# Kernel optimization log

Hardware: AMD Instinct MI355X
Metric: run time of the kernel (lower is better)

## Reference

```python
import jax, jax.numpy as jnp
import numpy as np

B, S, H, NH = 4, 2048, 2048, 16
HD = H // NH
EPS = 1e-5


def setup_inputs() -> dict:
    key = jax.random.key(0)
    ks = jax.random.split(key, 5)
    return {
        "x": jax.random.normal(ks[0], (B, S, H), dtype=jnp.float32),
        "ln_w": jnp.ones((H,), dtype=jnp.float32),
        "ln_b": jnp.zeros((H,), dtype=jnp.float32),
        "c_attn_w": jax.random.normal(ks[1], (H, 3 * H), dtype=jnp.float32) * 0.02,
        "c_attn_b": jax.random.normal(ks[2], (3 * H,), dtype=jnp.float32) * 0.02,
        "c_proj_w": jax.random.normal(ks[3], (H, H), dtype=jnp.float32) * 0.02,
        "c_proj_b": jax.random.normal(ks[4], (H,), dtype=jnp.float32) * 0.02,
    }


def reference(x, ln_w, ln_b, c_attn_w, c_attn_b, c_proj_w, c_proj_b):
    residual = x
    # fused layer norm
    mu = jnp.mean(x, axis=-1, keepdims=True)
    var = jnp.mean(jnp.square(x - mu), axis=-1, keepdims=True)
    xn = (x - mu) * jax.lax.rsqrt(var + EPS) * ln_w + ln_b
    qkv = jnp.einsum("bsh,hk->bsk", xn, c_attn_w) + c_attn_b
    q, k, v = jnp.split(qkv, 3, axis=-1)
    def heads(t):
        return t.reshape(B, S, NH, HD).transpose(0, 2, 1, 3)
    q, k, v = heads(q), heads(k), heads(v)
    # causal flash attention (reference math)
    scale = 1.0 / np.sqrt(HD)
    scores = jnp.einsum("bnqd,bnkd->bnqk", q, k) * scale
    causal = jnp.tril(jnp.ones((S, S), dtype=bool))
    scores = jnp.where(causal, scores, jnp.finfo(scores.dtype).min)
    attn = jax.nn.softmax(scores, axis=-1)
    o = jnp.einsum("bnqk,bnkd->bnqd", attn, v)
    # merge heads: [B,NH,S,HD] -> [B,S,H]
    o = o.transpose(0, 2, 1, 3).reshape(B, S, H)
    # output projection + residual (fused_ffn, add_gelu=False, dropout=0)
    return jnp.einsum("bsh,hk->bsk", o, c_proj_w) + c_proj_b + residual
```

## Files before the change

### kernel.cpp

```cpp
#include <hip/hip_runtime.h>
#include <stdint.h>
#include <math.h>

#define B_  4
#define S_  2048
#define H_  2048
#define NH_ 16
#define HD_ 128
#define M_  (B_*S_)
#define N3_ (3*H_)
#define NQT_ (S_/64)

typedef __attribute__((ext_vector_type(8))) short short8;
typedef __attribute__((ext_vector_type(4))) float floatx4;
typedef unsigned int u32;

__device__ __forceinline__ unsigned short f2bf(float f) {
  unsigned u = __float_as_uint(f);
  u += 0x7FFF + ((u >> 16) & 1);
  return (unsigned short)(u >> 16);
}

__device__ __forceinline__ void gl2lds16(const void* g, void* l) {
  __builtin_amdgcn_global_load_lds(
      (const __attribute__((address_space(1))) u32*)g,
      (__attribute__((address_space(3))) u32*)l, 16, 0, 0);
}

__global__ __launch_bounds__(256) void ln_kernel(
    const float* __restrict__ x, const float* __restrict__ w,
    const float* __restrict__ b, unsigned short* __restrict__ xn) {
  int row = blockIdx.x;
  int t = threadIdx.x;
  const float* xr = x + (size_t)row * H_;
  float4 v0 = *(const float4*)(xr + t * 4);
  float4 v1 = *(const float4*)(xr + 1024 + t * 4);
  float s  = v0.x + v0.y + v0.z + v0.w + v1.x + v1.y + v1.z + v1.w;
  float sq = v0.x*v0.x + v0.y*v0.y + v0.z*v0.z + v0.w*v0.w
           + v1.x*v1.x + v1.y*v1.y + v1.z*v1.z + v1.w*v1.w;
  #pragma unroll
  for (int m = 32; m; m >>= 1) { s += __shfl_xor(s, m); sq += __shfl_xor(sq, m); }
  __shared__ float red[8];
  int wv = t >> 6;
  if ((t & 63) == 0) { red[wv * 2] = s; red[wv * 2 + 1] = sq; }
  __syncthreads();
  s  = red[0] + red[2] + red[4] + red[6];
  sq = red[1] + red[3] + red[5] + red[7];
  float mu  = s * (1.0f / H_);
  float var = sq * (1.0f / H_) - mu * mu;
  float rs  = rsqrtf(var + 1e-5f);

  float4 w0 = *(const float4*)(w + t * 4);
  float4 b0 = *(const float4*)(b + t * 4);
  float4 w1 = *(const float4*)(w + 1024 + t * 4);
  float4 b1 = *(const float4*)(b + 1024 + t * 4);
  ushort4 o0, o1;
  o0.x = f2bf((v0.x - mu) * rs * w0.x + b0.x);
  o0.y = f2bf((v0.y - mu) * rs * w0.y + b0.y);
  o0.z = f2bf((v0.z - mu) * rs * w0.z + b0.z);
  o0.w = f2bf((v0.w - mu) * rs * w0.w + b0.w);
  o1.x = f2bf((v1.x - mu) * rs * w1.x + b1.x);
  o1.y = f2bf((v1.y - mu) * rs * w1.y + b1.y);
  o1.z = f2bf((v1.z - mu) * rs * w1.z + b1.z);
  o1.w = f2bf((v1.w - mu) * rs * w1.w + b1.w);
  unsigned short* orow = xn + (size_t)row * H_;
  *(ushort4*)(orow + t * 4) = o0;
  *(ushort4*)(orow + 1024 + t * 4) = o1;
}

__global__ __launch_bounds__(256) void transpose_f2b(
    const float* __restrict__ in, unsigned short* __restrict__ out,
    int R, int C) {
  __shared__ float tile[32][33];
  int tx = threadIdx.x & 31, ty = threadIdx.x >> 5;
  int c0 = blockIdx.x * 32, r0 = blockIdx.y * 32;
  #pragma unroll
  for (int i = 0; i < 32; i += 8)
    tile[ty + i][tx] = in[(size_t)(r0 + ty + i) * C + c0 + tx];
  __syncthreads();
  #pragma unroll
  for (int i = 0; i < 32; i += 8)
    out[(size_t)(c0 + ty + i) * R + r0 + tx] = f2bf(tile[tx][ty + i]);
}

__global__ __launch_bounds__(256) void qkv_gemm(
    const unsigned short* __restrict__ A, const unsigned short* __restrict__ Bt,
    const float* __restrict__ bias,
    unsigned short* __restrict__ qw, unsigned short* __restrict__ kw,
    unsigned short* __restrict__ vtw) {
  __shared__ unsigned short As[128 * 64];
  __shared__ unsigned short Bs[128 * 64];
  int n0 = blockIdx.x * 128, m0 = blockIdx.y * 128;
  int t = threadIdx.x, lane = t & 63, wv = t >> 6;
  int l15 = lane & 15, quad = lane >> 4;
  int wm = wv >> 1, wn = wv & 1;
  floatx4 acc[4][4];
  #pragma unroll
  for (int i = 0; i < 4; i++)
    #pragma unroll
    for (int j = 0; j < 4; j++) acc[i][j] = (floatx4){0.f, 0.f, 0.f, 0.f};

  const unsigned short* ag = A + (size_t)(m0 + (t >> 3)) * H_ + (t & 7) * 8;
  const unsigned short* bg = Bt + (size_t)(n0 + (t >> 3)) * H_ + (t & 7) * 8;
  unsigned short* asl = As + t * 8;
  unsigned short* bsl = Bs + t * 8;

  for (int k0 = 0; k0 < H_; k0 += 64) {
    __syncthreads();
    #pragma unroll
    for (int c = 0; c < 4; c++) {
      gl2lds16(ag + (size_t)(c * 32) * H_ + k0, asl + c * 2048);
      gl2lds16(bg + (size_t)(c * 32) * H_ + k0, bsl + c * 2048);
    }
    __syncthreads();
    #pragma unroll
    for (int ks = 0; ks < 2; ks++) {
      short8 af[4], bf[4];
      #pragma unroll
      for (int i = 0; i < 4; i++)
        af[i] = *(const short8*)(As + (wm * 64 + i * 16 + l15) * 64 + ks * 32 + quad * 8);
      #pragma unroll
      for (int j = 0; j < 4; j++)
        bf[j] = *(const short8*)(Bs + (wn * 64 + j * 16 + l15) * 64 + ks * 32 + quad * 8);
      #pragma unroll
      for (int i = 0; i < 4; i++)
        #pragma unroll
        for (int j = 0; j < 4; j++)
          acc[i][j] = __builtin_amdgcn_mfma_f32_16x16x32_bf16(af[i], bf[j], acc[i][j], 0, 0, 0);
    }
  }
  int sec = n0 >> 11;
  int h = (n0 >> 7) & 15;
  #pragma unroll
  for (int j = 0; j < 4; j++) {
    int d = wn * 64 + j * 16 + l15;
    float bval = bias[n0 + d];
    #pragma unroll
    for (int i = 0; i < 4; i++) {
      int m = m0 + wm * 64 + i * 16 + quad * 4;
      int bb = m >> 11, s = m & 2047;
      int bh = bb * NH_ + h;
      if (sec == 2) {
        ushort4 pv;
        pv.x = f2bf(acc[i][j][0] + bval); pv.y = f2bf(acc[i][j][1] + bval);
        pv.z = f2bf(acc[i][j][2] + bval); pv.w = f2bf(acc[i][j][3] + bval);
        *(ushort4*)(vtw + ((size_t)bh * HD_ + d) * S_ + s) = pv;
      } else {
        unsigned short* dst = (sec == 0 ? qw : kw) + ((size_t)bh * S_ + s) * HD_ + d;
        #pragma unroll
        for (int reg = 0; reg < 4; reg++)
          dst[(size_t)reg * HD_] = f2bf(acc[i][j][reg] + bval);
      }
    }
  }
}

__global__ __launch_bounds__(256) void proj_gemm(
    const unsigned short* __restrict__ A, const unsigned short* __restrict__ Bt,
    const float* __restrict__ bias, const float* __restrict__ resid,
    float* __restrict__ out) {
  __shared__ unsigned short As[128 * 64];
  __shared__ unsigned short Bs[128 * 64];
  int n0 = blockIdx.x * 128, m0 = blockIdx.y * 128;
  int t = threadIdx.x, lane = t & 63, wv = t >> 6;
  int l15 = lane & 15, quad = lane >> 4;
  int wm = wv >> 1, wn = wv & 1;
  floatx4 acc[4][4];
  #pragma unroll
  for (int i = 0; i < 4; i++)
    #pragma unroll
    for (int j = 0; j < 4; j++) acc[i][j] = (floatx4){0.f, 0.f, 0.f, 0.f};

  const unsigned short* ag = A + (size_t)(m0 + (t >> 3)) * H_ + (t & 7) * 8;
  const unsigned short* bg = Bt + (size_t)(n0 + (t >> 3)) * H_ + (t & 7) * 8;
  unsigned short* asl = As + t * 8;
  unsigned short* bsl = Bs + t * 8;

  for (int k0 = 0; k0 < H_; k0 += 64) {
    __syncthreads();
    #pragma unroll
    for (int c = 0; c < 4; c++) {
      gl2lds16(ag + (size_t)(c * 32) * H_ + k0, asl + c * 2048);
      gl2lds16(bg + (size_t)(c * 32) * H_ + k0, bsl + c * 2048);
    }
    __syncthreads();
    #pragma unroll
    for (int ks = 0; ks < 2; ks++) {
      short8 af[4], bf[4];
      #pragma unroll
      for (int i = 0; i < 4; i++)
        af[i] = *(const short8*)(As + (wm * 64 + i * 16 + l15) * 64 + ks * 32 + quad * 8);
      #pragma unroll
      for (int j = 0; j < 4; j++)
        bf[j] = *(const short8*)(Bs + (wn * 64 + j * 16 + l15) * 64 + ks * 32 + quad * 8);
      #pragma unroll
      for (int i = 0; i < 4; i++)
        #pragma unroll
        for (int j = 0; j < 4; j++)
          acc[i][j] = __builtin_amdgcn_mfma_f32_16x16x32_bf16(af[i], bf[j], acc[i][j], 0, 0, 0);
    }
  }
  #pragma unroll
  for (int j = 0; j < 4; j++) {
    int n = n0 + wn * 64 + j * 16 + l15;
    float bval = bias[n];
    #pragma unroll
    for (int i = 0; i < 4; i++) {
      #pragma unroll
      for (int reg = 0; reg < 4; reg++) {
        int m = m0 + wm * 64 + i * 16 + quad * 4 + reg;
        out[(size_t)m * H_ + n] = acc[i][j][reg] + bval + resid[(size_t)m * H_ + n];
      }
    }
  }
}

__global__ __launch_bounds__(256) void attn_kernel(
    const unsigned short* __restrict__ qw, const unsigned short* __restrict__ kw,
    const unsigned short* __restrict__ vtw, unsigned short* __restrict__ ow) {
  __shared__ unsigned short Klds[64 * 136];
  __shared__ unsigned short Vtl[128 * 72];
  __shared__ unsigned short Pl[4][16 * 72];
  int pr = blockIdx.x, bh = blockIdx.y;
  int t = threadIdx.x, lane = t & 63, wv = t >> 6;
  int l15 = lane & 15, quad = lane >> 4;
  int h = bh & 15, bb = bh >> 4;

  const float scale = 0.08838834764831845f;
  int krr = t >> 4, kcc = (t & 15) * 8;
  int vdd = t >> 3, vss = (t & 7) * 8;
  unsigned short* plw = &Pl[wv][0];
  const unsigned short* kgb = kw + ((size_t)bh * S_ + krr) * HD_ + kcc;
  const unsigned short* vgb = vtw + ((size_t)bh * HD_ + vdd) * S_ + vss;

  short8 kreg[4], vreg[4];
  auto load_stage = [&](int kb) {
    #pragma unroll
    for (int c = 0; c < 4; c++) {
      kreg[c] = *(const short8*)(kgb + (size_t)(kb + c * 16) * HD_);
      vreg[c] = *(const short8*)(vgb + (size_t)(c * 32) * S_ + kb);
    }
  };

  #pragma unroll 1
  for (int half = 0; half < 2; half++) {
    int qt = half ? (NQT_ - 1 - pr) : pr;
    int qr = qt * 64 + wv * 16;
    int q = qr + l15;

    short8 qf[4];
    {
      const unsigned short* qbase = qw + ((size_t)bh * S_ + q) * HD_ + quad * 8;
      #pragma unroll
      for (int ks = 0; ks < 4; ks++)
        qf[ks] = *(const short8*)(qbase + ks * 32);
    }

    float m_i = -INFINITY, l_i = 0.f;
    floatx4 o[8];
    #pragma unroll
    for (int ht = 0; ht < 8; ht++) o[ht] = (floatx4){0.f, 0.f, 0.f, 0.f};

    load_stage(0);
    #pragma unroll 1
    for (int kt = 0; kt <= qt; kt++) {
      int kb = kt * 64;
      __syncthreads();
      #pragma unroll
      for (int c = 0; c < 4; c++) {
        *(short8*)(Klds + (c * 16 + krr) * 136 + kcc) = kreg[c];
        *(short8*)(Vtl + (c * 32 + vdd) * 72 + vss) = vreg[c];
      }
      __syncthreads();
      if (kt < qt) load_stage(kb + 64);

      floatx4 sv[4];
      #pragma unroll
      for (int jm = 0; jm < 4; jm++) {
        sv[jm] = (floatx4){0.f, 0.f, 0.f, 0.f};
        #pragma unroll
        for (int ks = 0; ks < 4; ks++) {
          short8 kf = *(const short8*)(Klds + (jm * 16 + l15) * 136 + ks * 32 + quad * 8);
          sv[jm] = __builtin_amdgcn_mfma_f32_16x16x32_bf16(kf, qf[ks], sv[jm], 0, 0, 0);
        }
      }

      float p[4][4];
      float mx = m_i;
      #pragma unroll
      for (int jm = 0; jm < 4; jm++)
        #pragma unroll
        for (int reg = 0; reg < 4; reg++) {
          float v = sv[jm][reg] * scale;
          int key = kb + jm * 16 + quad * 4 + reg;
          if (key > q) v = -1e30f;
          p[jm][reg] = v;
          mx = fmaxf(mx, v);
        }
      mx = fmaxf(mx, __shfl_xor(mx, 16));
      mx = fmaxf(mx, __shfl_xor(mx, 32));
      float sum = 0.f;
      #pragma unroll
      for (int jm = 0; jm < 4; jm++)
        #pragma unroll
        for (int reg = 0; reg < 4; reg++) { p[jm][reg] = __expf(p[jm][reg] - mx); sum += p[jm][reg]; }
      sum += __shfl_xor(sum, 16);
      sum += __shfl_xor(sum, 32);
      float alpha = __expf(m_i - mx);
      l_i = l_i * alpha + sum;
      m_i = mx;
      #pragma unroll
      for (int ht = 0; ht < 8; ht++) o[ht] *= alpha;

      #pragma unroll
      for (int jm = 0; jm < 4; jm++) {
        ushort4 pk;
        pk.x = f2bf(p[jm][0]); pk.y = f2bf(p[jm][1]);
        pk.z = f2bf(p[jm][2]); pk.w = f2bf(p[jm][3]);
        *(ushort4*)(plw + l15 * 72 + jm * 16 + quad * 4) = pk;
      }

      #pragma unroll
      for (int ks2 = 0; ks2 < 2; ks2++) {
        short8 pf = *(const short8*)(plw + l15 * 72 + ks2 * 32 + quad * 8);
        #pragma unroll
        for (int ht = 0; ht < 8; ht++) {
          short8 vf = *(const short8*)(Vtl + (ht * 16 + l15) * 72 + ks2 * 32 + quad * 8);
          o[ht] = __builtin_amdgcn_mfma_f32_16x16x32_bf16(vf, pf, o[ht], 0, 0, 0);
        }
      }
    }

    float inv = 1.0f / l_i;
    size_t base = ((size_t)(bb * S_ + q)) * H_ + h * HD_ + quad * 4;
    #pragma unroll
    for (int ht = 0; ht < 8; ht++) {
      ushort4 ov;
      ov.x = f2bf(o[ht][0] * inv); ov.y = f2bf(o[ht][1] * inv);
      ov.z = f2bf(o[ht][2] * inv); ov.w = f2bf(o[ht][3] * inv);
      *(ushort4*)(ow + base + ht * 16) = ov;
    }
  }
}

extern "C" void kernel_launch(void* const* d_in, const int* in_sizes, int n_in,
                              void* d_out, int out_size, void* d_ws, size_t ws_size,
                              hipStream_t stream) {
  (void)in_sizes; (void)n_in; (void)out_size; (void)ws_size;
  const float* x      = (const float*)d_in[0];
  const float* ln_w   = (const float*)d_in[1];
  const float* ln_b   = (const float*)d_in[2];
  const float* attn_w = (const float*)d_in[3];
  const float* attn_b = (const float*)d_in[4];
  const float* proj_w = (const float*)d_in[5];
  const float* proj_b = (const float*)d_in[6];
  float* out = (float*)d_out;

  char* ws = (char*)d_ws;
  size_t off = 0;
  auto alloc = [&](size_t bytes) {
    char* p = ws + off;
    off += (bytes + 255) & ~(size_t)255;
    return p;
  };
  unsigned short* xn     = (unsigned short*)alloc((size_t)M_ * H_ * 2);
  unsigned short* wqkvt  = (unsigned short*)alloc((size_t)N3_ * H_ * 2);
  unsigned short* wprojt = (unsigned short*)alloc((size_t)H_ * H_ * 2);
  unsigned short* qws    = (unsigned short*)alloc((size_t)M_ * H_ * 2);
  unsigned short* kws    = (unsigned short*)alloc((size_t)M_ * H_ * 2);
  unsigned short* vtws   = (unsigned short*)alloc((size_t)M_ * H_ * 2);
  unsigned short* attn_out = xn;

  ln_kernel<<<M_, 256, 0, stream>>>(x, ln_w, ln_b, xn);
  transpose_f2b<<<dim3(N3_ / 32, H_ / 32), 256, 0, stream>>>(attn_w, wqkvt, H_, N3_);
  transpose_f2b<<<dim3(H_ / 32, H_ / 32), 256, 0, stream>>>(proj_w, wprojt, H_, H_);
  qkv_gemm<<<dim3(N3_ / 128, M_ / 128), 256, 0, stream>>>(xn, wqkvt, attn_b, qws, kws, vtws);
  attn_kernel<<<dim3(NQT_ / 2, B_ * NH_), 256, 0, stream>>>(qws, kws, vtws, attn_out);
  proj_gemm<<<dim3(H_ / 128, M_ / 128), 256, 0, stream>>>(attn_out, wprojt, proj_b, x, out);
}
```

Baseline: 729.9 us.

## Replace QKV and projection GEMMs with pipelined 256x256 swizzled LDS kernel

```diff
diff --git a/kernel.cpp b/kernel.cpp
--- a/kernel.cpp
+++ b/kernel.cpp
@@ -10,6 +10,7 @@
 #define M_  (B_*S_)
 #define N3_ (3*H_)
 #define NQT_ (S_/64)
+#define NT_ (H_/64)
 
 typedef __attribute__((ext_vector_type(8))) short short8;
 typedef __attribute__((ext_vector_type(4))) float floatx4;
@@ -83,61 +84,169 @@
     out[(size_t)(c0 + ty + i) * R + r0 + tx] = f2bf(tile[tx][ty + i]);
 }
 
-__global__ __launch_bounds__(256) void qkv_gemm(
+__device__ __forceinline__ void gemm256_acc(
+    const unsigned short* __restrict__ A, const unsigned short* __restrict__ Bt,
+    int m0, int n0, unsigned short (*sh)[16384], floatx4 (&acc)[8][4]) {
+  const int t = threadIdx.x;
+  const int lane = t & 63, wv = t >> 6;
+  const int l15 = lane & 15, quad = lane >> 4;
+  const int wm = wv >> 2, wn = wv & 3;
+  const int x7 = l15 & 7;
+
+  const int aRB = (wm * 128 + l15) * 64;
+  const int bRB = (wn * 64 + l15) * 64;
+  const int kx0 = ((0 + quad) ^ x7) * 8;
+  const int kx1 = ((4 + quad) ^ x7) * 8;
+
+  const int r = t >> 3, cc = t & 7;
+  const int scol = (cc ^ (r & 7)) * 8;
+  const unsigned short* aSrc = A + (size_t)(m0 + r) * H_ + scol;
+  const int btr = (r >> 5) * 64 + (r & 31);
+  const unsigned short* bSrc = Bt + (size_t)(n0 + btr) * H_ + scol;
+  const int aDst = t * 8;
+  const int bDst = (r >> 5) * 4096 + (r & 31) * 64 + cc * 8;
+
+  auto stageA = [&](int kt, int reg, int buf) {
+    const unsigned short* s = aSrc + (size_t)(reg * 64) * H_ + kt * 64;
+    unsigned short* d = sh[buf * 2] + aDst + reg * 4096;
+    gl2lds16(s, d);
+    gl2lds16(s + (size_t)128 * H_, d + 8192);
+  };
+  auto stageB = [&](int kt, int reg, int buf) {
+    const unsigned short* s = bSrc + (size_t)(reg * 32) * H_ + kt * 64;
+    unsigned short* d = sh[buf * 2 + 1] + bDst + reg * 2048;
+    gl2lds16(s, d);
+    gl2lds16(s + (size_t)128 * H_, d + 8192);
+  };
+
+  #pragma unroll
+  for (int i = 0; i < 8; i++)
+    #pragma unroll
+    for (int j = 0; j < 4; j++) acc[i][j] = (floatx4){0.f, 0.f, 0.f, 0.f};
+
+  stageA(0, 0, 0); stageB(0, 0, 0); stageA(0, 1, 0); stageB(0, 1, 0);
+  stageA(1, 0, 1); stageB(1, 0, 1); stageA(1, 1, 1);
+  asm volatile("s_waitcnt vmcnt(6)" ::: "memory");
+  __builtin_amdgcn_s_barrier();
+
+  short8 aR[4][2], b01[2][2], b23[2][2];
+
+  for (int n = 0; n < NT_; ++n) {
+    const int buf = n & 1;
+    const unsigned short* Ab = sh[buf * 2];
+    const unsigned short* Bb = sh[buf * 2 + 1];
+
+    #pragma unroll
+    for (int i = 0; i < 4; ++i) {
+      aR[i][0] = *(const short8*)(Ab + aRB + i * 1024 + kx0);
+      aR[i][1] = *(const short8*)(Ab + aRB + i * 1024 + kx1);
+    }
+    #pragma unroll
+    for (int j = 0; j < 2; ++j) {
+      b01[j][0] = *(const short8*)(Bb + bRB + j * 1024 + kx0);
+      b01[j][1] = *(const short8*)(Bb + bRB + j * 1024 + kx1);
+    }
+    if (n + 1 < NT_) stageB(n + 1, 1, buf ^ 1);
+    asm volatile("s_waitcnt lgkmcnt(8)" ::: "memory");
+    __builtin_amdgcn_s_barrier();
+    asm volatile("s_waitcnt lgkmcnt(0)" ::: "memory");
+    __builtin_amdgcn_sched_barrier(0);
+    __builtin_amdgcn_s_setprio(1);
+    #pragma unroll
+    for (int i = 0; i < 4; ++i)
+      #pragma unroll
+      for (int j = 0; j < 2; ++j) {
+        acc[i][j] = __builtin_amdgcn_mfma_f32_16x16x32_bf16(aR[i][0], b01[j][0], acc[i][j], 0, 0, 0);
+        acc[i][j] = __builtin_amdgcn_mfma_f32_16x16x32_bf16(aR[i][1], b01[j][1], acc[i][j], 0, 0, 0);
+      }
+    __builtin_amdgcn_s_setprio(0);
+    __builtin_amdgcn_s_barrier();
+
+    #pragma unroll
+    for (int j = 0; j < 2; ++j) {
+      b23[j][0] = *(const short8*)(Bb + bRB + (j + 2) * 1024 + kx0);
+      b23[j][1] = *(const short8*)(Bb + bRB + (j + 2) * 1024 + kx1);
+    }
+    if (n + 2 < NT_) stageA(n + 2, 0, buf);
+    __builtin_amdgcn_s_barrier();
+    asm volatile("s_waitcnt lgkmcnt(0)" ::: "memory");
+    __builtin_amdgcn_sched_barrier(0);
+    __builtin_amdgcn_s_setprio(1);
+    #pragma unroll
+    for (int i = 0; i < 4; ++i)
+      #pragma unroll
+      for (int j = 0; j < 2; ++j) {
+        acc[i][j + 2] = __builtin_amdgcn_mfma_f32_16x16x32_bf16(aR[i][0], b23[j][0], acc[i][j + 2], 0, 0, 0);
+        acc[i][j + 2] = __builtin_amdgcn_mfma_f32_16x16x32_bf16(aR[i][1], b23[j][1], acc[i][j + 2], 0, 0, 0);
+      }
+    __builtin_amdgcn_s_setprio(0);
+    __builtin_amdgcn_s_barrier();
+
+    #pragma unroll
+    for (int i = 0; i < 4; ++i) {
+      aR[i][0] = *(const short8*)(Ab + aRB + (i + 4) * 1024 + kx0);
+      aR[i][1] = *(const short8*)(Ab + aRB + (i + 4) * 1024 + kx1);
+    }
+    if (n + 2 < NT_) stageB(n + 2, 0, buf);
+    __builtin_amdgcn_s_barrier();
+    asm volatile("s_waitcnt lgkmcnt(0)" ::: "memory");
+    __builtin_amdgcn_sched_barrier(0);
+    __builtin_amdgcn_s_setprio(1);
+    #pragma unroll
+    for (int i = 0; i < 4; ++i)
+      #pragma unroll
+      for (int j = 0; j < 2; ++j) {
+        acc[i + 4][j] = __builtin_amdgcn_mfma_f32_16x16x32_bf16(aR[i][0], b01[j][0], acc[i + 4][j], 0, 0, 0);
+        acc[i + 4][j] = __builtin_amdgcn_mfma_f32_16x16x32_bf16(aR[i][1], b01[j][1], acc[i + 4][j], 0, 0, 0);
+      }
+    __builtin_amdgcn_s_setprio(0);
+    __builtin_amdgcn_s_barrier();
+
+    if (n + 2 < NT_) stageA(n + 2, 1, buf);
+    __builtin_amdgcn_s_barrier();
+    __builtin_amdgcn_s_setprio(1);
+    #pragma unroll
+    for (int i = 0; i < 4; ++i)
+      #pragma unroll
+      for (int j = 0; j < 2; ++j) {
+        acc[i + 4][j + 2] = __builtin_amdgcn_mfma_f32_16x16x32_bf16(aR[i][0], b23[j][0], acc[i + 4][j + 2], 0, 0, 0);
+        acc[i + 4][j + 2] = __builtin_amdgcn_mfma_f32_16x16x32_bf16(aR[i][1], b23[j][1], acc[i + 4][j + 2], 0, 0, 0);
+      }
+    __builtin_amdgcn_s_setprio(0);
+    if (n + 2 < NT_) asm volatile("s_waitcnt vmcnt(6)" ::: "memory");
+    else             asm volatile("s_waitcnt vmcnt(0)" ::: "memory");
+    __builtin_amdgcn_s_barrier();
+  }
+}
+
+__global__ __launch_bounds__(512, 2) void qkv_gemm(
     const unsigned short* __restrict__ A, const unsigned short* __restrict__ Bt,
     const float* __restrict__ bias,
     unsigned short* __restrict__ qw, unsigned short* __restrict__ kw,
     unsigned short* __restrict__ vtw) {
-  __shared__ unsigned short As[128 * 64];
-  __shared__ unsigned short Bs[128 * 64];
-  int n0 = blockIdx.x * 128, m0 = blockIdx.y * 128;
+  __shared__ unsigned short sh[4][16384];
+  int nwg = gridDim.x * gridDim.y;
+  int bid = blockIdx.y * gridDim.x + blockIdx.x;
+  int swz = (bid & 7) * (nwg >> 3) + (bid >> 3);
+  int n0 = (swz % gridDim.x) * 256;
+  int m0 = (swz / gridDim.x) * 256;
+
+  floatx4 acc[8][4];
+  gemm256_acc(A, Bt, m0, n0, sh, acc);
+
   int t = threadIdx.x, lane = t & 63, wv = t >> 6;
   int l15 = lane & 15, quad = lane >> 4;
-  int wm = wv >> 1, wn = wv & 1;
-  floatx4 acc[4][4];
-  #pragma unroll
-  for (int i = 0; i < 4; i++)
-    #pragma unroll
-    for (int j = 0; j < 4; j++) acc[i][j] = (floatx4){0.f, 0.f, 0.f, 0.f};
-
-  const unsigned short* ag = A + (size_t)(m0 + (t >> 3)) * H_ + (t & 7) * 8;
-  const unsigned short* bg = Bt + (size_t)(n0 + (t >> 3)) * H_ + (t & 7) * 8;
-  unsigned short* asl = As + t * 8;
-  unsigned short* bsl = Bs + t * 8;
-
-  for (int k0 = 0; k0 < H_; k0 += 64) {
-    __syncthreads();
-    #pragma unroll
-    for (int c = 0; c < 4; c++) {
-      gl2lds16(ag + (size_t)(c * 32) * H_ + k0, asl + c * 2048);
-      gl2lds16(bg + (size_t)(c * 32) * H_ + k0, bsl + c * 2048);
-    }
-    __syncthreads();
-    #pragma unroll
-    for (int ks = 0; ks < 2; ks++) {
-      short8 af[4], bf[4];
-      #pragma unroll
-      for (int i = 0; i < 4; i++)
-        af[i] = *(const short8*)(As + (wm * 64 + i * 16 + l15) * 64 + ks * 32 + quad * 8);
-      #pragma unroll
-      for (int j = 0; j < 4; j++)
-        bf[j] = *(const short8*)(Bs + (wn * 64 + j * 16 + l15) * 64 + ks * 32 + quad * 8);
-      #pragma unroll
-      for (int i = 0; i < 4; i++)
-        #pragma unroll
-        for (int j = 0; j < 4; j++)
-          acc[i][j] = __builtin_amdgcn_mfma_f32_16x16x32_bf16(af[i], bf[j], acc[i][j], 0, 0, 0);
-    }
-  }
+  int wm = wv >> 2, wn = wv & 3;
   int sec = n0 >> 11;
-  int h = (n0 >> 7) & 15;
-  #pragma unroll
-  for (int j = 0; j < 4; j++) {
-    int d = wn * 64 + j * 16 + l15;
-    float bval = bias[n0 + d];
-    #pragma unroll
-    for (int i = 0; i < 4; i++) {
-      int m = m0 + wm * 64 + i * 16 + quad * 4;
+  #pragma unroll
+  for (int j = 0; j < 4; ++j) {
+    int nn = n0 + wn * 64 + j * 16 + l15;
+    int h = (nn >> 7) & 15;
+    int d = nn & 127;
+    float bval = bias[nn];
+    #pragma unroll
+    for (int i = 0; i < 8; ++i) {
+      int m = m0 + wm * 128 + i * 16 + quad * 4;
       int bb = m >> 11, s = m & 2047;
       int bh = bb * NH_ + h;
       if (sec == 2) {
@@ -155,62 +264,34 @@
   }
 }
 
-__global__ __launch_bounds__(256) void proj_gemm(
+__global__ __launch_bounds__(512, 2) void proj_gemm(
     const unsigned short* __restrict__ A, const unsigned short* __restrict__ Bt,
     const float* __restrict__ bias, const float* __restrict__ resid,
     float* __restrict__ out) {
-  __shared__ unsigned short As[128 * 64];
-  __shared__ unsigned short Bs[128 * 64];
-  int n0 = blockIdx.x * 128, m0 = blockIdx.y * 128;
+  __shared__ unsigned short sh[4][16384];
+  int nwg = gridDim.x * gridDim.y;
+  int bid = blockIdx.y * gridDim.x + blockIdx.x;
+  int swz = (bid & 7) * (nwg >> 3) + (bid >> 3);
+  int n0 = (swz % gridDim.x) * 256;
+  int m0 = (swz / gridDim.x) * 256;
+
+  floatx4 acc[8][4];
+  gemm256_acc(A, Bt, m0, n0, sh, acc);
+
   int t = threadIdx.x, lane = t & 63, wv = t >> 6;
   int l15 = lane & 15, quad = lane >> 4;
-  int wm = wv >> 1, wn = wv & 1;
-  floatx4 acc[4][4];
-  #pragma unroll
-  for (int i = 0; i < 4; i++)
-    #pragma unroll
-    for (int j = 0; j < 4; j++) acc[i][j] = (floatx4){0.f, 0.f, 0.f, 0.f};
-
-  const unsigned short* ag = A + (size_t)(m0 + (t >> 3)) * H_ + (t & 7) * 8;
-  const unsigned short* bg = Bt + (size_t)(n0 + (t >> 3)) * H_ + (t & 7) * 8;
-  unsigned short* asl = As + t * 8;
-  unsigned short* bsl = Bs + t * 8;
-
-  for (int k0 = 0; k0 < H_; k0 += 64) {
-    __syncthreads();
-    #pragma unroll
-    for (int c = 0; c < 4; c++) {
-      gl2lds16(ag + (size_t)(c * 32) * H_ + k0, asl + c * 2048);
-      gl2lds16(bg + (size_t)(c * 32) * H_ + k0, bsl + c * 2048);
-    }
-    __syncthreads();
-    #pragma unroll
-    for (int ks = 0; ks < 2; ks++) {
-      short8 af[4], bf[4];
-      #pragma unroll
-      for (int i = 0; i < 4; i++)
-        af[i] = *(const short8*)(As + (wm * 64 + i * 16 + l15) * 64 + ks * 32 + quad * 8);
-      #pragma unroll
-      for (int j = 0; j < 4; j++)
-        bf[j] = *(const short8*)(Bs + (wn * 64 + j * 16 + l15) * 64 + ks * 32 + quad * 8);
-      #pragma unroll
-      for (int i = 0; i < 4; i++)
-        #pragma unroll
-        for (int j = 0; j < 4; j++)
-          acc[i][j] = __builtin_amdgcn_mfma_f32_16x16x32_bf16(af[i], bf[j], acc[i][j], 0, 0, 0);
-    }
-  }
-  #pragma unroll
-  for (int j = 0; j < 4; j++) {
-    int n = n0 + wn * 64 + j * 16 + l15;
-    float bval = bias[n];
-    #pragma unroll
-    for (int i = 0; i < 4; i++) {
-      #pragma unroll
-      for (int reg = 0; reg < 4; reg++) {
-        int m = m0 + wm * 64 + i * 16 + quad * 4 + reg;
-        out[(size_t)m * H_ + n] = acc[i][j][reg] + bval + resid[(size_t)m * H_ + n];
-      }
+  int wm = wv >> 2, wn = wv & 3;
+  #pragma unroll
+  for (int j = 0; j < 4; ++j) {
+    int nn = n0 + wn * 64 + j * 16 + l15;
+    float bval = bias[nn];
+    #pragma unroll
+    for (int i = 0; i < 8; ++i) {
+      int m = m0 + wm * 128 + i * 16 + quad * 4;
+      #pragma unroll
+      for (int reg = 0; reg < 4; ++reg)
+        out[(size_t)(m + reg) * H_ + nn] =
+            acc[i][j][reg] + bval + resid[(size_t)(m + reg) * H_ + nn];
     }
   }
 }
@@ -374,7 +455,7 @@
   ln_kernel<<<M_, 256, 0, stream>>>(x, ln_w, ln_b, xn);
   transpose_f2b<<<dim3(N3_ / 32, H_ / 32), 256, 0, stream>>>(attn_w, wqkvt, H_, N3_);
   transpose_f2b<<<dim3(H_ / 32, H_ / 32), 256, 0, stream>>>(proj_w, wprojt, H_, H_);
-  qkv_gemm<<<dim3(N3_ / 128, M_ / 128), 256, 0, stream>>>(xn, wqkvt, attn_b, qws, kws, vtws);
+  qkv_gemm<<<dim3(N3_ / 256, M_ / 256), 512, 0, stream>>>(xn, wqkvt, attn_b, qws, kws, vtws);
   attn_kernel<<<dim3(NQT_ / 2, B_ * NH_), 256, 0, stream>>>(qws, kws, vtws, attn_out);
-  proj_gemm<<<dim3(H_ / 128, M_ / 128), 256, 0, stream>>>(attn_out, wprojt, proj_b, x, out);
-}
+  proj_gemm<<<dim3(H_ / 256, M_ / 256), 512, 0, stream>>>(attn_out, wprojt, proj_b, x, out);
+}
```

Measured after the change: 619.0 us. 1.18x faster.
